# Kernel optimization log

Measured on AMD Instinct MI355X. Metric: run time of the kernel, lower is better.

Reference implementation:

```python
import jax
jax.config.update("jax_enable_x64", True)
import jax.numpy as jnp
import numpy as np
import math

B, L = 4, 4096
VOCAB, CVOCAB = 32000, 25000
HIDDEN, EDIM, NHEADS = 1024, 64, 8
NGRAMS = (2, 3)
TABLE_HINT = 100003
KSIZE, DILATION = 4, 3  # dilation = max ngram order
EPS = 1e-6


def _next_prime(n):
    if n <= 2:
        return 2
    c = n if n % 2 else n + 1
    while True:
        if all(c % i for i in range(3, int(math.isqrt(c)) + 1, 2)):
            return c
        c += 2


def _table_sizes():
    sizes, cur = [], TABLE_HINT
    for _ in range(NHEADS):
        p = _next_prime(cur)
        sizes.append(p)
        cur = p + 2
    return sizes


def setup_inputs():
    key = jax.random.key(0)
    ks = jax.random.split(key, 12)
    sizes = _table_sizes()  # identical for both ngram orders (same hint)
    max_s = max(sizes)
    n_orders = NGRAMS[1] - NGRAMS[0] + 1  # 2
    table_sizes = jnp.asarray(np.tile(np.array(sizes, dtype=np.int64), (n_orders, 1)))  # [2,8]
    tables = 0.01 * jax.random.normal(ks[0], (n_orders, NHEADS, max_s, EDIM), dtype=jnp.float32)
    return {
        "hidden_states": jax.random.normal(ks[1], (B, L, HIDDEN), dtype=jnp.float32),
        "token_ids": jax.random.randint(ks[2], (B, L), 0, VOCAB, dtype=jnp.int64),
        "projection": jax.random.randint(ks[3], (VOCAB,), 0, CVOCAB, dtype=jnp.int64),
        "mults2": jax.random.randint(ks[4], (NHEADS, 2), 1, 2**31 - 1, dtype=jnp.int64),
        "mults3": jax.random.randint(ks[5], (NHEADS, 3), 1, 2**31 - 1, dtype=jnp.int64),
        "table_sizes": table_sizes,
        "tables": tables,
        "w_k": (jax.random.normal(ks[6], (HIDDEN, n_orders * NHEADS * EDIM), dtype=jnp.float32) / math.sqrt(n_orders * NHEADS * EDIM)),
        "w_v": (jax.random.normal(ks[7], (HIDDEN, n_orders * NHEADS * EDIM), dtype=jnp.float32) / math.sqrt(n_orders * NHEADS * EDIM)),
        "q_norm_w": jnp.ones((HIDDEN,), dtype=jnp.float32),
        "k_norm_w": jnp.ones((HIDDEN,), dtype=jnp.float32),
        "conv_norm_w": jnp.ones((HIDDEN,), dtype=jnp.float32),
        "conv_w": 0.02 * jax.random.normal(ks[8], (HIDDEN, KSIZE), dtype=jnp.float32),
        "conv_b": jnp.zeros((HIDDEN,), dtype=jnp.float32),
    }


def _rmsnorm(x, w):
    norm = jax.lax.rsqrt(jnp.mean(jnp.square(x.astype(jnp.float32)), axis=-1, keepdims=True) + EPS)
    return (x.astype(jnp.float32) * norm).astype(x.dtype) * w


def _build_ngrams(compressed, n):
    # compressed: [B,L] int64 -> [B,L,n] causal windows with left zero pad
    p = jnp.pad(compressed, ((0, 0), (n - 1, 0)))
    return jnp.stack([p[:, i:i + compressed.shape[1]] for i in range(n)], axis=-1)


def _hash(ngrams, mults, sizes):
    # ngrams [B,L,n], mults [H,n], sizes [H] -> [B,L,H]
    prod = ngrams[:, :, None, :] * mults[None, None, :, :]  # int64
    mix = prod[..., 0]
    for i in range(1, prod.shape[-1]):
        mix = mix ^ prod[..., i]
    return jnp.abs(mix) % sizes[None, None, :]


def reference(hidden_states, token_ids, projection, mults2, mults3, table_sizes,
              tables, w_k, w_v, q_norm_w, k_norm_w, conv_norm_w, conv_w, conv_b):
    b, l, hidden = hidden_states.shape
    # ---- retrieve ----
    compressed = projection[jnp.clip(token_ids, 0, projection.shape[0] - 1)]  # [B,L]
    idx2 = _hash(_build_ngrams(compressed, 2), mults2, table_sizes[0])  # [B,L,H]
    idx3 = _hash(_build_ngrams(compressed, 3), mults3, table_sizes[1])  # [B,L,H]
    idx = jnp.concatenate([idx2, idx3], axis=-1)  # [B,L,2H] order: ngram2 heads, ngram3 heads
    n_tab = tables.shape[0] * tables.shape[1]
    tab_flat = tables.reshape(n_tab, tables.shape[2], tables.shape[3])
    emb = tab_flat[jnp.arange(n_tab), idx]  # [B,L,2H,EDIM] gather
    memory = emb.reshape(b, l, -1)  # [B,L,total_retrieval_dim]
    # ---- fuse ----
    k = jnp.einsum('bld,hd->blh', memory, w_k)
    v = jnp.einsum('bld,hd->blh', memory, w_v)
    q_n = _rmsnorm(hidden_states, q_norm_w)
    k_n = _rmsnorm(k, k_norm_w)
    scale = 1.0 / math.sqrt(hidden)
    gate = jax.nn.sigmoid(jnp.sum(q_n * k_n, axis=-1, keepdims=True) * scale)
    v_g = gate * v
    # ---- short conv (causal depthwise, dilation=3, kernel=4) ----
    h = _rmsnorm(v_g, conv_norm_w)
    pad = (KSIZE - 1) * DILATION  # 9; right padding is sliced off by [..., :L]
    hp = jnp.pad(h, ((0, 0), (pad, 0), (0, 0)))
    y = conv_b
    for j in range(KSIZE):
        y = y + hp[:, j * DILATION: j * DILATION + l, :] * conv_w[None, None, :, j]
    return jax.nn.silu(y) + v_g


if __name__ == "__main__":
    out = reference(**setup_inputs())
    print(out.shape, out.dtype)
```

## Files before the change

### kernel.cpp

```cpp
#include <hip/hip_runtime.h>
#include <hip/hip_bf16.h>
#include <math.h>

typedef unsigned short u16;
typedef __bf16 bf16x8 __attribute__((ext_vector_type(8)));
typedef float f32x4 __attribute__((ext_vector_type(4)));
typedef unsigned short u16x4 __attribute__((ext_vector_type(4)));
typedef unsigned short u16x8 __attribute__((ext_vector_type(8)));

#define BB 4
#define LL 4096
#define MTOK (BB*LL)
#define HID 1024
#define NKV 2048
#define KDIM 1024
#define VOCABN 32000
#define EPSF 1e-6f

__device__ __forceinline__ float bf2f(u16 x) {
  unsigned u = ((unsigned)x) << 16;
  return __builtin_bit_cast(float, u);
}
__device__ __forceinline__ u16 f2bf(float f) {
  unsigned u = __builtin_bit_cast(unsigned, f);
  u += 0x7FFFu + ((u >> 16) & 1u);
  return (u16)(u >> 16);
}

__global__ __launch_bounds__(256) void k_convert_w(const float* __restrict__ wk,
                                                   const float* __restrict__ wv,
                                                   u16* __restrict__ W) {
  int i = blockIdx.x * 256 + threadIdx.x;
  const int n4 = (NKV * KDIM) / 4;
  if (i >= n4) return;
  const int half = n4 / 2;
  const f32x4* src = (i < half) ? (const f32x4*)wk : (const f32x4*)wv;
  int j = (i < half) ? i : i - half;
  f32x4 v = src[j];
  u16x4 o = { f2bf(v[0]), f2bf(v[1]), f2bf(v[2]), f2bf(v[3]) };
  *(u16x4*)&W[(size_t)i * 4] = o;
}

__global__ __launch_bounds__(256) void k_gather(
    const int* __restrict__ tok, const int* __restrict__ proj,
    const int* __restrict__ m2, const int* __restrict__ m3,
    const int* __restrict__ tsz, const float* __restrict__ tables,
    int max_s, u16* __restrict__ mem) {
  int m = blockIdx.x;
  int l = m & (LL - 1);
  int tid = threadIdx.x;
  int t = tid >> 4;
  int q = tid & 15;
  long long c0, c1 = 0, c2 = 0;
  {
    int tk = tok[m];
    tk = tk < 0 ? 0 : (tk > VOCABN - 1 ? VOCABN - 1 : tk);
    c0 = proj[tk];
  }
  if (l >= 1) {
    int tk = tok[m - 1];
    tk = tk < 0 ? 0 : (tk > VOCABN - 1 ? VOCABN - 1 : tk);
    c1 = proj[tk];
  }
  if (l >= 2) {
    int tk = tok[m - 2];
    tk = tk < 0 ? 0 : (tk > VOCABN - 1 ? VOCABN - 1 : tk);
    c2 = proj[tk];
  }
  int order = t >> 3, h = t & 7;
  long long mix;
  if (order == 0) {
    mix = (c1 * (long long)m2[h * 2 + 0]) ^ (c0 * (long long)m2[h * 2 + 1]);
  } else {
    mix = (c2 * (long long)m3[h * 3 + 0]) ^ (c1 * (long long)m3[h * 3 + 1]) ^
          (c0 * (long long)m3[h * 3 + 2]);
  }
  unsigned long long um = (unsigned long long)(mix < 0 ? -mix : mix);
  unsigned long long usz = (unsigned long long)tsz[t];
  unsigned long long qq = (unsigned long long)((double)um / (double)usz);
  long long r = (long long)(um - qq * usz);
  if (r < 0) r += (long long)usz;
  else if (r >= (long long)usz) r -= (long long)usz;
  const f32x4* src = (const f32x4*)(tables + ((size_t)t * (size_t)max_s + (size_t)r) * 64);
  f32x4 e = src[q];
  u16x4 o = { f2bf(e[0]), f2bf(e[1]), f2bf(e[2]), f2bf(e[3]) };
  *(u16x4*)&mem[(size_t)m * HID + t * 64 + q * 4] = o;
}

#define GBK2 32
#define BUF2 32768

__device__ __forceinline__ void gload16(const void* g, void* l) {
  __builtin_amdgcn_global_load_lds((__attribute__((address_space(1))) void*)(g),
                                   (__attribute__((address_space(3))) void*)(l), 16, 0, 0);
}
__device__ __forceinline__ int swz32(int x) { return x ^ (((x >> 6) & 3) << 4); }

__global__ __launch_bounds__(512, 2) void k_gemm(const u16* __restrict__ A,
                                                 const u16* __restrict__ Bw,
                                                 u16* __restrict__ C) {
  __shared__ __align__(16) char lds[131072];
  const int d = blockIdx.x;
  const int wg = (d & 7) * 64 + (d >> 3);
  const int bm = wg >> 3, bn = wg & 7;
  const int tid = threadIdx.x;
  const int w = tid >> 6, lane = tid & 63;
  const int wm = w >> 2, wn = w & 3;
  const int lm = lane & 15, kg = lane >> 4;

  const int ca0 = w * 2, ca1 = w * 2 + 1;
  const int row0 = ca0 * 16 + (lane >> 2);
  const int row1 = ca1 * 16 + (lane >> 2);
  const int off0 = row0 * KDIM + (((lane & 3) ^ (row0 & 3)) << 3);
  const int off1 = row1 * KDIM + (((lane & 3) ^ (row1 & 3)) << 3);
  const int dstA0 = ca0 * 1024 + lane * 16;
  const int dstA1 = ca1 * 1024 + lane * 16;
  const u16* Ap = A + (size_t)bm * 256 * KDIM;
  const u16* Bp = Bw + (size_t)bn * 256 * KDIM;

  int aro[8], bro[4];
#pragma unroll
  for (int mi = 0; mi < 8; ++mi)
    aro[mi] = swz32((wm * 128 + mi * 16 + lm) * 64 + kg * 16);
#pragma unroll
  for (int ni = 0; ni < 4; ++ni)
    bro[ni] = 16384 + swz32((wn * 64 + ni * 16 + lm) * 64 + kg * 16);

  f32x4 acc[8][4];
#pragma unroll
  for (int i = 0; i < 8; ++i)
#pragma unroll
    for (int j = 0; j < 4; ++j) acc[i][j] = (f32x4){0.f, 0.f, 0.f, 0.f};

#define STG(kt, bb)                                                        \
  {                                                                        \
    char* bbase = lds + (bb) * BUF2;                                       \
    gload16(Ap + off0 + (kt) * GBK2, bbase + dstA0);                       \
    gload16(Bp + off0 + (kt) * GBK2, bbase + 16384 + dstA0);               \
    gload16(Ap + off1 + (kt) * GBK2, bbase + dstA1);                       \
    gload16(Bp + off1 + (kt) * GBK2, bbase + 16384 + dstA1);               \
  }

#define TILE(t, bb, VMS, DOSTG)                                            \
  {                                                                        \
    asm volatile("s_waitcnt vmcnt(" VMS ")" ::: "memory");                 \
    __builtin_amdgcn_s_barrier();                                          \
    if (DOSTG) STG((t) + 3, ((bb) + 3) & 3);                               \
    const char* buf = lds + (bb) * BUF2;                                   \
    bf16x8 af[8], bf[4];                                                   \
    _Pragma("unroll")                                                      \
    for (int mi = 0; mi < 8; ++mi) af[mi] = *(const bf16x8*)(buf + aro[mi]); \
    _Pragma("unroll")                                                      \
    for (int ni = 0; ni < 4; ++ni) bf[ni] = *(const bf16x8*)(buf + bro[ni]); \
    asm volatile("s_waitcnt lgkmcnt(0)" ::: "memory");                     \
    __builtin_amdgcn_sched_barrier(0);                                     \
    __builtin_amdgcn_s_setprio(1);                                         \
    _Pragma("unroll")                                                      \
    for (int mi = 0; mi < 8; ++mi)                                         \
      _Pragma("unroll")                                                    \
      for (int ni = 0; ni < 4; ++ni)                                       \
        acc[mi][ni] = __builtin_amdgcn_mfma_f32_16x16x32_bf16(af[mi], bf[ni], acc[mi][ni], 0, 0, 0); \
    __builtin_amdgcn_s_setprio(0);                                         \
  }

  STG(0, 0);
  STG(1, 1);
  STG(2, 2);
#pragma unroll 1
  for (int t4 = 0; t4 < 7; ++t4) {
    const int t = t4 * 4;
    TILE(t + 0, 0, "8", 1);
    TILE(t + 1, 1, "8", 1);
    TILE(t + 2, 2, "8", 1);
    TILE(t + 3, 3, "8", 1);
  }
  TILE(28, 0, "8", 1);
  TILE(29, 1, "8", 0);
  TILE(30, 2, "4", 0);
  TILE(31, 3, "0", 0);
#undef STG
#undef TILE

  __syncthreads();
  u16* tile = (u16*)lds;
#pragma unroll
  for (int mi = 0; mi < 8; ++mi)
#pragma unroll
    for (int ni = 0; ni < 4; ++ni)
#pragma unroll
      for (int jj = 0; jj < 4; ++jj) {
        int r = wm * 128 + mi * 16 + kg * 4 + jj;
        int ccol = wn * 64 + ni * 16 + lm;
        tile[r * 256 + ccol] = f2bf(acc[mi][ni][jj]);
      }
  __syncthreads();
#pragma unroll
  for (int it = 0; it < 8; ++it) {
    int r = it * 32 + (tid >> 4);
    int cb = (tid & 15) * 32;
    *(f32x4*)((char*)C + ((size_t)(bm * 256 + r) * NKV + bn * 256) * 2 + cb) =
        *(const f32x4*)((char*)tile + r * 512 + cb);
    *(f32x4*)((char*)C + ((size_t)(bm * 256 + r) * NKV + bn * 256) * 2 + cb + 16) =
        *(const f32x4*)((char*)tile + r * 512 + cb + 16);
  }
}

#define CR 32

__global__ __launch_bounds__(256, 2) void k_gateconv(
    const float* __restrict__ hidden, const u16* __restrict__ KV,
    const float* __restrict__ qw, const float* __restrict__ kw,
    const float* __restrict__ cw, const float* __restrict__ convw,
    const float* __restrict__ convb, float* __restrict__ out) {
  __shared__ u16 ring[32][1024];
  const int blk = blockIdx.x;
  const int b = blk >> 7;
  const int l0 = (blk & 127) * CR;
  const int w = threadIdx.x >> 6, ln = threadIdx.x & 63;

  float qk[16], cwv[16];
  f32x4 wt[16];
  f32x4 cbv[4];
#pragma unroll
  for (int seg = 0; seg < 2; ++seg) {
    int c0 = seg * 512 + ln * 8;
    f32x4 qa = *(const f32x4*)&qw[c0], qb = *(const f32x4*)&qw[c0 + 4];
    f32x4 ka = *(const f32x4*)&kw[c0], kb = *(const f32x4*)&kw[c0 + 4];
    f32x4 ca = *(const f32x4*)&cw[c0], cbx = *(const f32x4*)&cw[c0 + 4];
#pragma unroll
    for (int i = 0; i < 4; ++i) {
      qk[seg * 8 + i] = qa[i] * ka[i];
      qk[seg * 8 + 4 + i] = qb[i] * kb[i];
      cwv[seg * 8 + i] = ca[i];
      cwv[seg * 8 + 4 + i] = cbx[i];
    }
    cbv[seg * 2] = *(const f32x4*)&convb[c0];
    cbv[seg * 2 + 1] = *(const f32x4*)&convb[c0 + 4];
#pragma unroll
    for (int e = 0; e < 8; ++e) wt[seg * 8 + e] = *(const f32x4*)&convw[(c0 + e) * 4];
  }

  const int base = l0 - 12;
  f32x4 x0, x1, x2, x3, nx0, nx1, nx2, nx3;
  u16x8 kk0, kk1, vv0, vv1, nk0, nk1, nv0, nv1;

#define LOADROW(r, X0, X1, X2, X3, K0, K1, V0, V1)                             \
  {                                                                            \
    X0 = (f32x4){0.f,0.f,0.f,0.f}; X1 = X0; X2 = X0; X3 = X0;                  \
    K0 = (u16x8){0,0,0,0,0,0,0,0}; K1 = K0; V0 = K0; V1 = K0;                  \
    if ((r) >= l0 - 9 && (r) >= 0) {                                           \
      size_t mr = (size_t)b * LL + (r);                                        \
      X0 = *(const f32x4*)&hidden[mr * HID + ln * 8];                          \
      X1 = *(const f32x4*)&hidden[mr * HID + ln * 8 + 4];                      \
      X2 = *(const f32x4*)&hidden[mr * HID + 512 + ln * 8];                    \
      X3 = *(const f32x4*)&hidden[mr * HID + 512 + ln * 8 + 4];                \
      K0 = *(const u16x8*)&KV[mr * NKV + ln * 8];                              \
      K1 = *(const u16x8*)&KV[mr * NKV + 512 + ln * 8];                        \
      V0 = *(const u16x8*)&KV[mr * NKV + HID + ln * 8];                        \
      V1 = *(const u16x8*)&KV[mr * NKV + HID + 512 + ln * 8];                  \
    }                                                                          \
  }

  LOADROW(base + w, x0, x1, x2, x3, kk0, kk1, vv0, vv1);

#pragma unroll 1
  for (int g = 0; g < 11; ++g) {
    const int r = base + g * 4 + w;
    if (g < 10) {
      LOADROW(r + 4, nx0, nx1, nx2, nx3, nk0, nk1, nv0, nv1);
    }
    float s0 = 0.f, s1 = 0.f, s2 = 0.f, s3 = 0.f;
#pragma unroll
    for (int e = 0; e < 8; ++e) {
      float xa = (e < 4) ? x0[e] : x1[e - 4];
      float xb = (e < 4) ? x2[e] : x3[e - 4];
      float ka = bf2f(kk0[e]), kb = bf2f(kk1[e]);
      float va = bf2f(vv0[e]), vb = bf2f(vv1[e]);
      s0 += xa * xa + xb * xb;
      s1 += ka * ka + kb * kb;
      s2 += xa * qk[e] * ka + xb * qk[8 + e] * kb;
      s3 += va * va + vb * vb;
    }
#pragma unroll
    for (int mm = 32; mm >= 1; mm >>= 1) {
      s0 += __shfl_xor(s0, mm, 64);
      s1 += __shfl_xor(s1, mm, 64);
      s2 += __shfl_xor(s2, mm, 64);
      s3 += __shfl_xor(s3, mm, 64);
    }
    const float inv = 0.0009765625f;
    float rq = rsqrtf(s0 * inv + EPSF);
    float rk = rsqrtf(s1 * inv + EPSF);
    float gate = 1.f / (1.f + expf(-rq * rk * s2 * 0.03125f));
    float rv = rsqrtf(gate * gate * s3 * inv + EPSF);
    float grv = gate * rv;

    u16x8 h0p, h1p;
#pragma unroll
    for (int e = 0; e < 8; ++e) {
      h0p[e] = f2bf(bf2f(vv0[e]) * grv * cwv[e]);
      h1p[e] = f2bf(bf2f(vv1[e]) * grv * cwv[8 + e]);
    }
    const int slot = r & 31;
    *(u16x8*)&ring[slot][ln * 8] = h0p;
    *(u16x8*)&ring[slot][512 + ln * 8] = h1p;
    __syncthreads();

    if (r >= l0) {
      const int s9 = (r - 9) & 31, s6 = (r - 6) & 31, s3s = (r - 3) & 31;
      size_t mr = (size_t)b * LL + r;
#pragma unroll
      for (int seg = 0; seg < 2; ++seg) {
        u16x8 a9 = *(const u16x8*)&ring[s9][seg * 512 + ln * 8];
        u16x8 a6 = *(const u16x8*)&ring[s6][seg * 512 + ln * 8];
        u16x8 a3 = *(const u16x8*)&ring[s3s][seg * 512 + ln * 8];
        const u16x8 vv = seg ? vv1 : vv0;
        f32x4 ra, rb;
#pragma unroll
        for (int e = 0; e < 8; ++e) {
          const int idx = seg * 8 + e;
          float vf = bf2f(vv[e]);
          float hown = vf * grv * cwv[idx];
          f32x4 wv = wt[idx];
          float y = cbv[seg * 2 + (e >> 2)][e & 3] + bf2f(a9[e]) * wv[0] +
                    bf2f(a6[e]) * wv[1] + bf2f(a3[e]) * wv[2] + hown * wv[3];
          float res = y / (1.f + expf(-y)) + gate * vf;
          if (e < 4) ra[e] = res; else rb[e - 4] = res;
        }
        *(f32x4*)&out[mr * HID + seg * 512 + ln * 8] = ra;
        *(f32x4*)&out[mr * HID + seg * 512 + ln * 8 + 4] = rb;
      }
    }
    x0 = nx0; x1 = nx1; x2 = nx2; x3 = nx3;
    kk0 = nk0; kk1 = nk1; vv0 = nv0; vv1 = nv1;
  }
#undef LOADROW
}

extern "C" void kernel_launch(void* const* d_in, const int* in_sizes, int n_in,
                              void* d_out, int out_size, void* d_ws, size_t ws_size,
                              hipStream_t stream) {
  const float* hidden   = (const float*)d_in[0];
  const int*   tok      = (const int*)d_in[1];
  const int*   proj     = (const int*)d_in[2];
  const int*   m2       = (const int*)d_in[3];
  const int*   m3       = (const int*)d_in[4];
  const int*   tsz      = (const int*)d_in[5];
  const float* tables   = (const float*)d_in[6];
  const float* wk       = (const float*)d_in[7];
  const float* wv       = (const float*)d_in[8];
  const float* qw       = (const float*)d_in[9];
  const float* kw       = (const float*)d_in[10];
  const float* cnw      = (const float*)d_in[11];
  const float* convw    = (const float*)d_in[12];
  const float* convb    = (const float*)d_in[13];
  float* out = (float*)d_out;

  const int max_s = in_sizes[6] / (2 * 8 * 64);

  char* ws = (char*)d_ws;
  u16* mem = (u16*)ws;
  u16* W   = (u16*)(ws + (size_t)33554432);
  u16* KV  = (u16*)(ws + (size_t)33554432 + 4194304);

  k_convert_w<<<dim3((NKV * KDIM / 4 + 255) / 256), dim3(256), 0, stream>>>(wk, wv, W);
  k_gather<<<dim3(MTOK), dim3(256), 0, stream>>>(tok, proj, m2, m3, tsz, tables, max_s, mem);
  k_gemm<<<dim3((MTOK / 256) * (NKV / 256)), dim3(512), 0, stream>>>(mem, W, KV);
  k_gateconv<<<dim3(BB * (LL / CR)), dim3(256), 0, stream>>>(hidden, KV, qw, kw, cnw, convw, convb, out);
}
```

Before: 160.5 us.

## Batch gather per block, split GEMM staging, move conv weights to LDS

Three separate changes. The gather kernel now has each block handle 16 tokens: it computes the 256 hash indices in parallel, shares them through LDS, and then loops over heads, which cuts the number of blocks and the redundant token and projection loads. The GEMM splits each k-tile into two halves of A fragments, with A and B prefetches issued between them and an extra barrier added. The gate/conv kernel shrinks its ring buffer to 16 slots and moves the conv weights from registers into a swizzled LDS array so it can run at occupancy 3. In return it adds a per-row __syncthreads, which is needed now that the ring is shorter.

```diff
diff --git a/kernel.cpp b/kernel.cpp
--- a/kernel.cpp
+++ b/kernel.cpp
@@ -46,11 +46,14 @@
     const int* __restrict__ m2, const int* __restrict__ m3,
     const int* __restrict__ tsz, const float* __restrict__ tables,
     int max_s, u16* __restrict__ mem) {
-  int m = blockIdx.x;
-  int l = m & (LL - 1);
-  int tid = threadIdx.x;
-  int t = tid >> 4;
-  int q = tid & 15;
+  __shared__ int sidx[16][16];
+  const int m0 = blockIdx.x * 16;
+  const int tid = threadIdx.x;
+  const int tt = tid >> 4;
+  const int t = tid & 15;
+  const int m = m0 + tt;
+  const int l = m & (LL - 1);
+
   long long c0, c1 = 0, c2 = 0;
   {
     int tk = tok[m];
@@ -81,10 +84,18 @@
   long long r = (long long)(um - qq * usz);
   if (r < 0) r += (long long)usz;
   else if (r >= (long long)usz) r -= (long long)usz;
-  const f32x4* src = (const f32x4*)(tables + ((size_t)t * (size_t)max_s + (size_t)r) * 64);
-  f32x4 e = src[q];
-  u16x4 o = { f2bf(e[0]), f2bf(e[1]), f2bf(e[2]), f2bf(e[3]) };
-  *(u16x4*)&mem[(size_t)m * HID + t * 64 + q * 4] = o;
+  sidx[tt][t] = (int)r;
+  __syncthreads();
+
+  const int q = t;
+#pragma unroll
+  for (int it = 0; it < 16; ++it) {
+    int idx = sidx[tt][it];
+    const f32x4* src = (const f32x4*)(tables + ((size_t)it * (size_t)max_s + (size_t)idx) * 64);
+    f32x4 e = src[q];
+    u16x4 o = { f2bf(e[0]), f2bf(e[1]), f2bf(e[2]), f2bf(e[3]) };
+    *(u16x4*)&mem[(size_t)m * HID + it * 64 + q * 4] = o;
+  }
 }
 
 #define GBK2 32
@@ -132,12 +143,16 @@
 #pragma unroll
     for (int j = 0; j < 4; ++j) acc[i][j] = (f32x4){0.f, 0.f, 0.f, 0.f};
 
-#define STG(kt, bb)                                                        \
+#define STGA(kt, bb)                                                       \
   {                                                                        \
     char* bbase = lds + (bb) * BUF2;                                       \
     gload16(Ap + off0 + (kt) * GBK2, bbase + dstA0);                       \
+    gload16(Ap + off1 + (kt) * GBK2, bbase + dstA1);                       \
+  }
+#define STGB(kt, bb)                                                       \
+  {                                                                        \
+    char* bbase = lds + (bb) * BUF2;                                       \
     gload16(Bp + off0 + (kt) * GBK2, bbase + 16384 + dstA0);               \
-    gload16(Ap + off1 + (kt) * GBK2, bbase + dstA1);                       \
     gload16(Bp + off1 + (kt) * GBK2, bbase + 16384 + dstA1);               \
   }
 
@@ -145,27 +160,40 @@
   {                                                                        \
     asm volatile("s_waitcnt vmcnt(" VMS ")" ::: "memory");                 \
     __builtin_amdgcn_s_barrier();                                          \
-    if (DOSTG) STG((t) + 3, ((bb) + 3) & 3);                               \
     const char* buf = lds + (bb) * BUF2;                                   \
-    bf16x8 af[8], bf[4];                                                   \
+    bf16x8 af0[4], bfr[4], af1[4];                                         \
     _Pragma("unroll")                                                      \
-    for (int mi = 0; mi < 8; ++mi) af[mi] = *(const bf16x8*)(buf + aro[mi]); \
+    for (int mi = 0; mi < 4; ++mi) af0[mi] = *(const bf16x8*)(buf + aro[mi]); \
     _Pragma("unroll")                                                      \
-    for (int ni = 0; ni < 4; ++ni) bf[ni] = *(const bf16x8*)(buf + bro[ni]); \
+    for (int ni = 0; ni < 4; ++ni) bfr[ni] = *(const bf16x8*)(buf + bro[ni]); \
+    if (DOSTG) STGA((t) + 3, ((bb) + 3) & 3);                              \
     asm volatile("s_waitcnt lgkmcnt(0)" ::: "memory");                     \
     __builtin_amdgcn_sched_barrier(0);                                     \
     __builtin_amdgcn_s_setprio(1);                                         \
     _Pragma("unroll")                                                      \
-    for (int mi = 0; mi < 8; ++mi)                                         \
+    for (int mi = 0; mi < 4; ++mi)                                         \
       _Pragma("unroll")                                                    \
       for (int ni = 0; ni < 4; ++ni)                                       \
-        acc[mi][ni] = __builtin_amdgcn_mfma_f32_16x16x32_bf16(af[mi], bf[ni], acc[mi][ni], 0, 0, 0); \
+        acc[mi][ni] = __builtin_amdgcn_mfma_f32_16x16x32_bf16(af0[mi], bfr[ni], acc[mi][ni], 0, 0, 0); \
     __builtin_amdgcn_s_setprio(0);                                         \
-  }
-
-  STG(0, 0);
-  STG(1, 1);
-  STG(2, 2);
+    __builtin_amdgcn_s_barrier();                                          \
+    _Pragma("unroll")                                                      \
+    for (int mi = 0; mi < 4; ++mi) af1[mi] = *(const bf16x8*)(buf + aro[4 + mi]); \
+    if (DOSTG) STGB((t) + 3, ((bb) + 3) & 3);                              \
+    asm volatile("s_waitcnt lgkmcnt(0)" ::: "memory");                     \
+    __builtin_amdgcn_sched_barrier(0);                                     \
+    __builtin_amdgcn_s_setprio(1);                                         \
+    _Pragma("unroll")                                                      \
+    for (int mi = 0; mi < 4; ++mi)                                         \
+      _Pragma("unroll")                                                    \
+      for (int ni = 0; ni < 4; ++ni)                                       \
+        acc[4 + mi][ni] = __builtin_amdgcn_mfma_f32_16x16x32_bf16(af1[mi], bfr[ni], acc[4 + mi][ni], 0, 0, 0); \
+    __builtin_amdgcn_s_setprio(0);                                         \
+  }
+
+  STGA(0, 0); STGB(0, 0);
+  STGA(1, 1); STGB(1, 1);
+  STGA(2, 2); STGB(2, 2);
 #pragma unroll 1
   for (int t4 = 0; t4 < 7; ++t4) {
     const int t = t4 * 4;
@@ -178,7 +206,8 @@
   TILE(29, 1, "8", 0);
   TILE(30, 2, "4", 0);
   TILE(31, 3, "0", 0);
-#undef STG
+#undef STGA
+#undef STGB
 #undef TILE
 
   __syncthreads();
@@ -207,19 +236,28 @@
 
 #define CR 32
 
-__global__ __launch_bounds__(256, 2) void k_gateconv(
+__global__ __launch_bounds__(256, 3) void k_gateconv(
     const float* __restrict__ hidden, const u16* __restrict__ KV,
     const float* __restrict__ qw, const float* __restrict__ kw,
     const float* __restrict__ cw, const float* __restrict__ convw,
     const float* __restrict__ convb, float* __restrict__ out) {
-  __shared__ u16 ring[32][1024];
+  __shared__ u16 ring[16][1024];
+  __shared__ f32x4 cwt[1024];
   const int blk = blockIdx.x;
   const int b = blk >> 7;
   const int l0 = (blk & 127) * CR;
   const int w = threadIdx.x >> 6, ln = threadIdx.x & 63;
 
+  {
+    const f32x4* cw4 = (const f32x4*)convw;
+#pragma unroll
+    for (int j = 0; j < 4; ++j) {
+      int i = threadIdx.x * 4 + j;
+      cwt[i ^ ((i >> 3) & 7)] = cw4[i];
+    }
+  }
+
   float qk[16], cwv[16];
-  f32x4 wt[16];
   f32x4 cbv[4];
 #pragma unroll
   for (int seg = 0; seg < 2; ++seg) {
@@ -236,9 +274,8 @@
     }
     cbv[seg * 2] = *(const f32x4*)&convb[c0];
     cbv[seg * 2 + 1] = *(const f32x4*)&convb[c0 + 4];
-#pragma unroll
-    for (int e = 0; e < 8; ++e) wt[seg * 8 + e] = *(const f32x4*)&convw[(c0 + e) * 4];
-  }
+  }
+  __syncthreads();
 
   const int base = l0 - 12;
   f32x4 x0, x1, x2, x3, nx0, nx1, nx2, nx3;
@@ -301,13 +338,13 @@
       h0p[e] = f2bf(bf2f(vv0[e]) * grv * cwv[e]);
       h1p[e] = f2bf(bf2f(vv1[e]) * grv * cwv[8 + e]);
     }
-    const int slot = r & 31;
+    const int slot = r & 15;
     *(u16x8*)&ring[slot][ln * 8] = h0p;
     *(u16x8*)&ring[slot][512 + ln * 8] = h1p;
     __syncthreads();
 
     if (r >= l0) {
-      const int s9 = (r - 9) & 31, s6 = (r - 6) & 31, s3s = (r - 3) & 31;
+      const int s9 = (r - 9) & 15, s6 = (r - 6) & 15, s3s = (r - 3) & 15;
       size_t mr = (size_t)b * LL + r;
 #pragma unroll
       for (int seg = 0; seg < 2; ++seg) {
@@ -321,7 +358,8 @@
           const int idx = seg * 8 + e;
           float vf = bf2f(vv[e]);
           float hown = vf * grv * cwv[idx];
-          f32x4 wv = wt[idx];
+          int wi = seg * 512 + ln * 8 + e;
+          f32x4 wv = cwt[wi ^ ((wi >> 3) & 7)];
           float y = cbv[seg * 2 + (e >> 2)][e & 3] + bf2f(a9[e]) * wv[0] +
                     bf2f(a6[e]) * wv[1] + bf2f(a3[e]) * wv[2] + hown * wv[3];
           float res = y / (1.f + expf(-y)) + gate * vf;
@@ -331,6 +369,7 @@
         *(f32x4*)&out[mr * HID + seg * 512 + ln * 8 + 4] = rb;
       }
     }
+    __syncthreads();
     x0 = nx0; x1 = nx1; x2 = nx2; x3 = nx3;
     kk0 = nk0; kk1 = nk1; vv0 = nv0; vv1 = nv1;
   }
@@ -364,7 +403,7 @@
   u16* KV  = (u16*)(ws + (size_t)33554432 + 4194304);
 
   k_convert_w<<<dim3((NKV * KDIM / 4 + 255) / 256), dim3(256), 0, stream>>>(wk, wv, W);
-  k_gather<<<dim3(MTOK), dim3(256), 0, stream>>>(tok, proj, m2, m3, tsz, tables, max_s, mem);
+  k_gather<<<dim3(MTOK / 16), dim3(256), 0, stream>>>(tok, proj, m2, m3, tsz, tables, max_s, mem);
   k_gemm<<<dim3((MTOK / 256) * (NKV / 256)), dim3(512), 0, stream>>>(mem, W, KV);
   k_gateconv<<<dim3(BB * (LL / CR)), dim3(256), 0, stream>>>(hidden, KV, qw, kw, cnw, convw, convb, out);
 }
```

Result: no change. 161.6 us (+0.7%).
